# Performance work log

Measured on AMD Instinct MI355X. Metric: run time of the kernel, lower is better.

The kernel has to match this reference:

```python
import jax, jax.numpy as jnp
from jax import lax
import numpy as np

DN = ('NCHW', 'OIHW', 'NCHW')

def _conv(x, w, b):
    y = lax.conv_general_dilated(x, w, (1, 1), 'VALID', dimension_numbers=DN)
    return y + b[None, :, None, None]

def _prelu(x, a):
    return jnp.where(x >= 0, x, a[None, :, None, None] * x)

def _maxpool2(x):
    # MaxPool2d(2,2,ceil_mode=True); spatial dims chosen even so VALID matches.
    return lax.reduce_window(x, -jnp.inf, lax.max, (1, 1, 2, 2), (1, 1, 2, 2), 'VALID')

def setup_inputs() -> dict:
    key = jax.random.key(0)
    ks = jax.random.split(key, 16)
    f = jnp.float32
    x = jax.random.uniform(ks[0], (16, 3, 720, 720), dtype=f) * 255.0
    def w(k, shape, fan_in):
        return jax.random.normal(k, shape, dtype=f) * (1.0 / np.sqrt(fan_in))
    return {
        'x': x,
        'conv1_w': w(ks[1], (10, 3, 3, 3), 27), 'conv1_b': jnp.zeros((10,), f),
        'prelu1_a': jnp.full((10,), 0.25, f),
        'conv2_w': w(ks[2], (16, 10, 3, 3), 90), 'conv2_b': jnp.zeros((16,), f),
        'prelu2_a': jnp.full((16,), 0.25, f),
        'conv3_w': w(ks[3], (32, 16, 3, 3), 144), 'conv3_b': jnp.zeros((32,), f),
        'prelu3_a': jnp.full((32,), 0.25, f),
        'conv41_w': w(ks[4], (2, 32, 1, 1), 32), 'conv41_b': jnp.zeros((2,), f),
        'conv42_w': w(ks[5], (4, 32, 1, 1), 32), 'conv42_b': jnp.zeros((4,), f),
    }

def reference(x, conv1_w, conv1_b, prelu1_a, conv2_w, conv2_b, prelu2_a,
              conv3_w, conv3_b, prelu3_a, conv41_w, conv41_b, conv42_w, conv42_b):
    # MTCNN pixel normalization from detect_p_net
    h = (x - 127.5) * 0.0078125
    h = _prelu(_conv(h, conv1_w, conv1_b), prelu1_a)   # [B,10,718,718]
    h = _maxpool2(h)                                   # [B,10,359,359]
    h = _prelu(_conv(h, conv2_w, conv2_b), prelu2_a)   # [B,16,357,357]
    h = _prelu(_conv(h, conv3_w, conv3_b), prelu3_a)   # [B,32,355,355]
    prob = jax.nn.softmax(_conv(h, conv41_w, conv41_b), axis=1)  # [B,2,355,355]
    reg = _conv(h, conv42_w, conv42_b)                            # [B,4,355,355]
    return (reg, prob)
```

## Files before the change

### kernel.cpp

```cpp
#include <hip/hip_runtime.h>
#include <hip/hip_bf16.h>
#include <cstddef>


#define H1 718
#define PH 359
#define H2 357
#define H3 355

#define W1R_OFF 0
#define B1R_OFF 288
#define AW2_OFF 320
#define BW3_OFF 1600
#define P16_OFF 4096
#define C2H_OFF 16500864

typedef short bf16x8 __attribute__((ext_vector_type(8)));
typedef float f32x4  __attribute__((ext_vector_type(4)));
typedef float f32x16 __attribute__((ext_vector_type(16)));
typedef unsigned short ushort4v __attribute__((ext_vector_type(4)));

__global__ void repack_kernel(const float* __restrict__ w1, const float* __restrict__ b1,
                              const float* __restrict__ w2, const float* __restrict__ w3,
                              float* __restrict__ ws) {
    int t = threadIdx.x;
    const float S = 0.0078125f;
    for (int i = t; i < 270; i += blockDim.x) ws[W1R_OFF + i] = w1[i] * S;
    if (t < 10) {
        float s = 0.f;
        for (int i = 0; i < 27; i++) s += w1[t * 27 + i];
        ws[B1R_OFF + t] = b1[t] - 127.5f * S * s;
    }
    unsigned short* aw2 = (unsigned short*)(ws + AW2_OFF);
    for (int e = t; e < 2560; e += blockDim.x) {
        int s = e >> 9;
        int rem = e & 511;
        int l = rem >> 3, j = rem & 7;
        int q = l >> 4, co = l & 15;
        int tap = 2 * s + (q >> 1);
        int ci  = ((q & 1) << 3) + j;
        float v = (tap < 9 && ci < 10) ? w2[co * 90 + ci * 9 + tap] : 0.f;
        __hip_bfloat16 h = __float2bfloat16(v);
        aw2[e] = *(unsigned short*)&h;
    }
    unsigned short* bw3 = (unsigned short*)(ws + BW3_OFF);
    for (int e = t; e < 4608; e += blockDim.x) {
        int tap = e >> 9;
        int rem = e & 511;
        int l = rem >> 3, j = rem & 7;
        int kh = tap / 3, kw = tap % 3;
        int co = l & 31, ci = ((l >> 5) << 3) + j;
        float v = w3[co * 144 + ci * 9 + kh * 3 + kw];
        __hip_bfloat16 h = __float2bfloat16(v);
        bw3[e] = *(unsigned short*)&h;
    }
}

__global__ void conv1_pool_kernel(const float* __restrict__ x,
                                  const float* __restrict__ ws,
                                  const float* __restrict__ a1,
                                  __hip_bfloat16* __restrict__ p16) {
    int pw = blockIdx.x * blockDim.x + threadIdx.x;
    int ph = blockIdx.y;
    int n  = blockIdx.z;
    if (pw >= PH) return;
    int iy = 2 * ph, ix = 2 * pw;

    float acc[10][4];
    #pragma unroll
    for (int c = 0; c < 10; c++)
        #pragma unroll
        for (int p = 0; p < 4; p++) acc[c][p] = 0.f;

    #pragma unroll
    for (int ci = 0; ci < 3; ci++) {
        const float* xp = x + (((size_t)(n * 3 + ci) * 720 + iy) * 720 + ix);
        float win[4][4];
        #pragma unroll
        for (int r = 0; r < 4; r++) {
            float2 v0 = *(const float2*)(xp + r * 720);
            float2 v1 = *(const float2*)(xp + r * 720 + 2);
            win[r][0] = v0.x; win[r][1] = v0.y; win[r][2] = v1.x; win[r][3] = v1.y;
        }
        #pragma unroll
        for (int c = 0; c < 10; c++) {
            const float* wk = ws + W1R_OFF + c * 27 + ci * 9;
            #pragma unroll
            for (int kh = 0; kh < 3; kh++)
                #pragma unroll
                for (int kw = 0; kw < 3; kw++) {
                    float wv = wk[kh * 3 + kw];
                    acc[c][0] = fmaf(win[kh    ][kw    ], wv, acc[c][0]);
                    acc[c][1] = fmaf(win[kh    ][kw + 1], wv, acc[c][1]);
                    acc[c][2] = fmaf(win[kh + 1][kw    ], wv, acc[c][2]);
                    acc[c][3] = fmaf(win[kh + 1][kw + 1], wv, acc[c][3]);
                }
        }
    }

    __hip_bfloat16 o[16];
    #pragma unroll
    for (int c = 0; c < 10; c++) {
        float b = ws[B1R_OFF + c], al = a1[c];
        float s0 = acc[c][0] + b, s1 = acc[c][1] + b;
        float s2 = acc[c][2] + b, s3 = acc[c][3] + b;
        s0 = s0 >= 0.f ? s0 : al * s0;
        s1 = s1 >= 0.f ? s1 : al * s1;
        s2 = s2 >= 0.f ? s2 : al * s2;
        s3 = s3 >= 0.f ? s3 : al * s3;
        o[c] = __float2bfloat16(fmaxf(fmaxf(s0, s1), fmaxf(s2, s3)));
    }
    #pragma unroll
    for (int c = 10; c < 16; c++) o[c] = __float2bfloat16(0.f);

    float4* dst = (float4*)(p16 + (((size_t)n * PH + ph) * PH + pw) * 16);
    dst[0] = ((float4*)o)[0];
    dst[1] = ((float4*)o)[1];
}

__global__ __launch_bounds__(256)
void conv2_mfma_kernel(const __hip_bfloat16* __restrict__ p16,
                       const float* __restrict__ ws,
                       const float* __restrict__ b2,
                       const float* __restrict__ a2,
                       __hip_bfloat16* __restrict__ c2h) {
    int wv = threadIdx.x >> 6;
    int l  = threadIdx.x & 63;
    int oh  = blockIdx.y * 4 + wv;
    int ow0 = blockIdx.x * 64;
    int n   = blockIdx.z;
    if (oh >= H2) return;

    int pxl = l & 15;
    int q   = l >> 4;
    int taph = q >> 1;
    int choff = (q & 1) << 3;

    const bf16x8* aw = (const bf16x8*)(ws + AW2_OFF);
    bf16x8 afr[5];
    #pragma unroll
    for (int s = 0; s < 5; s++) afr[s] = aw[s * 64 + l];

    bf16x8 zf;
    #pragma unroll
    for (int j = 0; j < 8; j++) zf[j] = 0;

    f32x4 acc[4];
    #pragma unroll
    for (int t = 0; t < 4; t++)
        #pragma unroll
        for (int i = 0; i < 4; i++) acc[t][i] = 0.f;

    #pragma unroll
    for (int s = 0; s < 5; s++) {
        int tap = 2 * s + taph;
        bool real = (tap < 9);
        int kh = tap / 3, kw = tap - kh * 3;
        int ih = oh + kh; if (ih > PH - 1) ih = PH - 1;
        #pragma unroll
        for (int t = 0; t < 4; t++) {
            int iw = ow0 + t * 16 + pxl + kw; if (iw > PH - 1) iw = PH - 1;
            const bf16x8* bp = (const bf16x8*)(p16 + (((size_t)n * PH + ih) * PH + iw) * 16 + choff);
            bf16x8 b = real ? *bp : zf;
            acc[t] = __builtin_amdgcn_mfma_f32_16x16x32_bf16(afr[s], b, acc[t], 0, 0, 0);
        }
    }

    float bb[4], aa[4];
    #pragma unroll
    for (int r = 0; r < 4; r++) { bb[r] = b2[q * 4 + r]; aa[r] = a2[q * 4 + r]; }

    #pragma unroll
    for (int t = 0; t < 4; t++) {
        int px = ow0 + t * 16 + pxl;
        if (px < H2) {
            ushort4v pk;
            #pragma unroll
            for (int r = 0; r < 4; r++) {
                float v = acc[t][r] + bb[r];
                v = v >= 0.f ? v : aa[r] * v;
                __hip_bfloat16 h = __float2bfloat16(v);
                pk[r] = *(unsigned short*)&h;
            }
            *(ushort4v*)(c2h + (((size_t)n * H2 + oh) * H2 + px) * 16 + q * 4) = pk;
        }
    }
}

__global__ __launch_bounds__(256, 1)
void conv3_heads_kernel(const __hip_bfloat16* __restrict__ c2h,
                        const float* __restrict__ ws,
                        const float* __restrict__ b3,
                        const float* __restrict__ a3,
                        const float* __restrict__ w41,
                        const float* __restrict__ b41,
                        const float* __restrict__ w42,
                        const float* __restrict__ b42,
                        float* __restrict__ out) {
    int wv = threadIdx.x >> 6;
    int l  = threadIdx.x & 63;
    int ow0 = blockIdx.x * 32;
    int oh0 = blockIdx.y * 8 + wv * 2;
    int n   = blockIdx.z;

    int m    = l & 31;
    int half = l >> 5;
    int choff = half << 3;

    const bf16x8* bw = (const bf16x8*)(ws + BW3_OFF);
    bf16x8 bfr[9];
    #pragma unroll
    for (int t = 0; t < 9; t++) bfr[t] = bw[t * 64 + l];

    f32x16 acc0, acc1;
    #pragma unroll
    for (int i = 0; i < 16; i++) { acc0[i] = 0.f; acc1[i] = 0.f; }

    #pragma unroll
    for (int kh = 0; kh < 3; kh++) {
        int ih0 = oh0 + kh;     if (ih0 > H2 - 1) ih0 = H2 - 1;
        int ih1 = oh0 + 1 + kh; if (ih1 > H2 - 1) ih1 = H2 - 1;
        #pragma unroll
        for (int kw = 0; kw < 3; kw++) {
            int iw = ow0 + m + kw; if (iw > H2 - 1) iw = H2 - 1;
            const bf16x8* a0p = (const bf16x8*)(c2h + ((((size_t)n * H2 + ih0) * H2 + iw) << 4) + choff);
            const bf16x8* a1p = (const bf16x8*)(c2h + ((((size_t)n * H2 + ih1) * H2 + iw) << 4) + choff);
            bf16x8 a0 = *a0p;
            bf16x8 a1 = *a1p;
            int tap = kh * 3 + kw;
            acc0 = __builtin_amdgcn_mfma_f32_32x32x16_bf16(a0, bfr[tap], acc0, 0, 0, 0);
            acc1 = __builtin_amdgcn_mfma_f32_32x32x16_bf16(a1, bfr[tap], acc1, 0, 0, 0);
        }
    }

    __shared__ float hbuf[4][64 * 33];
    float* hb = hbuf[wv];
    float bb = b3[m], aa = a3[m];
    #pragma unroll
    for (int t = 0; t < 2; t++) {
        #pragma unroll
        for (int r = 0; r < 16; r++) {
            int mprime = (r & 3) + ((r >> 2) << 3) + (half << 2);
            float v = (t ? acc1[r] : acc0[r]) + bb;
            v = v >= 0.f ? v : aa * v;
            hb[(t * 32 + mprime) * 33 + m] = v;
        }
    }
    __syncthreads();

    int poh = oh0 + (l >> 5);
    int pow_ = ow0 + (l & 31);
    float h[32];
    #pragma unroll
    for (int c = 0; c < 32; c++) h[c] = hb[l * 33 + c];

    float l0 = b41[0], l1 = b41[1];
    float r0 = b42[0], r1 = b42[1], r2 = b42[2], r3 = b42[3];
    #pragma unroll
    for (int c = 0; c < 32; c++) {
        float hv = h[c];
        l0 = fmaf(hv, w41[c],      l0);
        l1 = fmaf(hv, w41[32 + c], l1);
        r0 = fmaf(hv, w42[c],      r0);
        r1 = fmaf(hv, w42[32 + c], r1);
        r2 = fmaf(hv, w42[64 + c], r2);
        r3 = fmaf(hv, w42[96 + c], r3);
    }
    float mx  = fmaxf(l0, l1);
    float e0 = __expf(l0 - mx), e1 = __expf(l1 - mx);
    float inv = 1.0f / (e0 + e1);

    if (poh < H3 && pow_ < H3) {
        const size_t sp = (size_t)H3 * H3;
        size_t pos = (size_t)poh * H3 + pow_;
        float* reg  = out;
        float* prob = out + (size_t)16 * 4 * sp;
        reg[((size_t)(n * 4 + 0)) * sp + pos] = r0;
        reg[((size_t)(n * 4 + 1)) * sp + pos] = r1;
        reg[((size_t)(n * 4 + 2)) * sp + pos] = r2;
        reg[((size_t)(n * 4 + 3)) * sp + pos] = r3;
        prob[((size_t)(n * 2 + 0)) * sp + pos] = e0 * inv;
        prob[((size_t)(n * 2 + 1)) * sp + pos] = e1 * inv;
    }
}

extern "C" void kernel_launch(void* const* d_in, const int* in_sizes, int n_in,
                              void* d_out, int out_size, void* d_ws, size_t ws_size,
                              hipStream_t stream) {
    const float* x   = (const float*)d_in[0];
    const float* w1  = (const float*)d_in[1];
    const float* b1  = (const float*)d_in[2];
    const float* a1  = (const float*)d_in[3];
    const float* w2  = (const float*)d_in[4];
    const float* b2  = (const float*)d_in[5];
    const float* a2  = (const float*)d_in[6];
    const float* w3  = (const float*)d_in[7];
    const float* b3  = (const float*)d_in[8];
    const float* a3  = (const float*)d_in[9];
    const float* w41 = (const float*)d_in[10];
    const float* b41 = (const float*)d_in[11];
    const float* w42 = (const float*)d_in[12];
    const float* b42 = (const float*)d_in[13];
    float* out = (float*)d_out;
    float* ws  = (float*)d_ws;

    __hip_bfloat16* p16 = (__hip_bfloat16*)(ws + P16_OFF);
    __hip_bfloat16* c2h = (__hip_bfloat16*)(ws + C2H_OFF);

    repack_kernel<<<1, 256, 0, stream>>>(w1, b1, w2, w3, ws);

    {
        dim3 grid((PH + 127) / 128, PH, 16);
        conv1_pool_kernel<<<grid, 128, 0, stream>>>(x, ws, a1, p16);
    }
    {
        dim3 grid((H2 + 63) / 64, (H2 + 3) / 4, 16);
        conv2_mfma_kernel<<<grid, 256, 0, stream>>>(p16, ws, b2, a2, c2h);
    }
    {
        dim3 grid((H3 + 31) / 32, (H3 + 7) / 8, 16);
        conv3_heads_kernel<<<grid, 256, 0, stream>>>(c2h, ws, b3, a3,
                                                     w41, b41, w42, b42, out);
    }
}
```

Before: 316.6 us.

## Run conv1+PReLU+maxpool on bf16 MFMA with LDS-staged input tile

Replaces the per-thread scalar-FMA conv1/PReLU/pool kernel with a tiled kernel. Each block stages a 66x18 input tile into shared memory, converting the three channels to bf16. It then computes the 3x3 conv as nine 32x32x16 bf16 MFMAs per row pair, using pre-scaled bf16 weights from an extended repack. PReLU and 2x2 max-pooling are fused in registers. The aim is to move conv1 off the vector ALUs. In exchange, most of the MFMA K and N lanes are padding, the raw pixel input is rounded to bf16, and outputs are written as scattered 2-byte stores. The padding channels 10-15 of the pooled buffer are also no longer explicitly zeroed.

Measured after the change: 348.6 us. 10.1% more time.

```diff
diff --git a/kernel.cpp b/kernel.cpp
--- a/kernel.cpp
+++ b/kernel.cpp
@@ -8,28 +8,43 @@
 #define H2 357
 #define H3 355
 
-#define W1R_OFF 0
-#define B1R_OFF 288
-#define AW2_OFF 320
-#define BW3_OFF 1600
-#define P16_OFF 4096
-#define C2H_OFF 16500864
+#define B1R_OFF 0
+#define BW1_OFF 16
+#define AW2_OFF 2320
+#define BW3_OFF 3600
+#define P16_OFF 5952
+#define C2H_OFF 16502720
 
 typedef short bf16x8 __attribute__((ext_vector_type(8)));
 typedef float f32x4  __attribute__((ext_vector_type(4)));
 typedef float f32x16 __attribute__((ext_vector_type(16)));
 typedef unsigned short ushort4v __attribute__((ext_vector_type(4)));
+
+static __device__ __forceinline__ bf16x8 make_a(uint2 q) {
+    union { unsigned int u[4]; bf16x8 v; } c;
+    c.u[0] = q.x; c.u[1] = q.y; c.u[2] = q.x; c.u[3] = q.y;
+    return c.v;
+}
 
 __global__ void repack_kernel(const float* __restrict__ w1, const float* __restrict__ b1,
                               const float* __restrict__ w2, const float* __restrict__ w3,
                               float* __restrict__ ws) {
     int t = threadIdx.x;
     const float S = 0.0078125f;
-    for (int i = t; i < 270; i += blockDim.x) ws[W1R_OFF + i] = w1[i] * S;
     if (t < 10) {
         float s = 0.f;
         for (int i = 0; i < 27; i++) s += w1[t * 27 + i];
         ws[B1R_OFF + t] = b1[t] - 127.5f * S * s;
+    }
+    unsigned short* bw1 = (unsigned short*)(ws + BW1_OFF);
+    for (int e = t; e < 4608; e += blockDim.x) {
+        int tap = e >> 9;
+        int rem = e & 511;
+        int l = rem >> 3, j = rem & 7;
+        int n = l & 31, k = ((l >> 5) << 3) + j;
+        float v = (k < 3 && n < 10) ? w1[n * 27 + k * 9 + tap] * S : 0.f;
+        __hip_bfloat16 h = __float2bfloat16(v);
+        bw1[e] = *(unsigned short*)&h;
     }
     unsigned short* aw2 = (unsigned short*)(ws + AW2_OFF);
     for (int e = t; e < 2560; e += blockDim.x) {
@@ -56,66 +71,82 @@
     }
 }
 
-__global__ void conv1_pool_kernel(const float* __restrict__ x,
-                                  const float* __restrict__ ws,
-                                  const float* __restrict__ a1,
-                                  __hip_bfloat16* __restrict__ p16) {
-    int pw = blockIdx.x * blockDim.x + threadIdx.x;
-    int ph = blockIdx.y;
+__global__ __launch_bounds__(256)
+void conv1_mfma_kernel(const float* __restrict__ x,
+                       const float* __restrict__ ws,
+                       const float* __restrict__ a1,
+                       __hip_bfloat16* __restrict__ p16) {
+    __shared__ uint2 st[18][68];
+    int tid = threadIdx.x;
+    int wv = tid >> 6;
+    int l  = tid & 63;
+    int x0 = blockIdx.x * 64;
+    int y0 = blockIdx.y * 16;
     int n  = blockIdx.z;
-    if (pw >= PH) return;
-    int iy = 2 * ph, ix = 2 * pw;
-
-    float acc[10][4];
-    #pragma unroll
-    for (int c = 0; c < 10; c++)
-        #pragma unroll
-        for (int p = 0; p < 4; p++) acc[c][p] = 0.f;
-
-    #pragma unroll
-    for (int ci = 0; ci < 3; ci++) {
-        const float* xp = x + (((size_t)(n * 3 + ci) * 720 + iy) * 720 + ix);
-        float win[4][4];
-        #pragma unroll
-        for (int r = 0; r < 4; r++) {
-            float2 v0 = *(const float2*)(xp + r * 720);
-            float2 v1 = *(const float2*)(xp + r * 720 + 2);
-            win[r][0] = v0.x; win[r][1] = v0.y; win[r][2] = v1.x; win[r][3] = v1.y;
-        }
-        #pragma unroll
-        for (int c = 0; c < 10; c++) {
-            const float* wk = ws + W1R_OFF + c * 27 + ci * 9;
+
+    for (int e = tid; e < 66 * 18; e += 256) {
+        int row = e / 66, xx = e - row * 66;
+        int gx = x0 + xx; if (gx > 719) gx = 719;
+        int gy = y0 + row; if (gy > 719) gy = 719;
+        const float* xp = x + (size_t)n * 1555200 + (size_t)gy * 720 + gx;
+        __hip_bfloat16 h0 = __float2bfloat16(xp[0]);
+        __hip_bfloat16 h1 = __float2bfloat16(xp[518400]);
+        __hip_bfloat16 h2 = __float2bfloat16(xp[1036800]);
+        uint2 val;
+        val.x = (unsigned int)(*(unsigned short*)&h0) |
+                ((unsigned int)(*(unsigned short*)&h1) << 16);
+        val.y = (unsigned int)(*(unsigned short*)&h2);
+        st[row][xx] = val;
+    }
+    __syncthreads();
+
+    const bf16x8* bw = (const bf16x8*)(ws + BW1_OFF);
+    bf16x8 bfr[9];
+    #pragma unroll
+    for (int t = 0; t < 9; t++) bfr[t] = bw[t * 64 + l];
+
+    int lm = l & 31, half = l >> 5;
+    float bch = (lm < 10) ? ws[B1R_OFF + lm] : 0.f;
+    float ach = (lm < 10) ? a1[lm] : 0.f;
+
+    #pragma unroll
+    for (int pr = 0; pr < 2; pr++) {
+        int ly  = (wv << 2) + (pr << 1);
+        int phg = (y0 + ly) >> 1;
+        #pragma unroll
+        for (int t = 0; t < 2; t++) {
+            f32x16 acc0, acc1;
             #pragma unroll
-            for (int kh = 0; kh < 3; kh++)
+            for (int i = 0; i < 16; i++) { acc0[i] = 0.f; acc1[i] = 0.f; }
+            int bx = (t << 5) + lm;
+            #pragma unroll
+            for (int tap = 0; tap < 9; tap++) {
+                int kh = tap / 3, kw = tap - kh * 3;
+                uint2 q0 = st[ly + kh][bx + kw];
+                uint2 q1 = st[ly + kh + 1][bx + kw];
+                acc0 = __builtin_amdgcn_mfma_f32_32x32x16_bf16(make_a(q0), bfr[tap], acc0, 0, 0, 0);
+                acc1 = __builtin_amdgcn_mfma_f32_32x32x16_bf16(make_a(q1), bfr[tap], acc1, 0, 0, 0);
+            }
+            float pv[16];
+            #pragma unroll
+            for (int r = 0; r < 16; r++) {
+                float v0 = acc0[r] + bch; v0 = fmaxf(v0, ach * v0);
+                float v1 = acc1[r] + bch; v1 = fmaxf(v1, ach * v1);
+                pv[r] = fmaxf(v0, v1);
+            }
+            if (lm < 10 && phg < PH) {
+                size_t rowbase = (((size_t)n * PH + phg) * PH) * 16 + lm;
                 #pragma unroll
-                for (int kw = 0; kw < 3; kw++) {
-                    float wv = wk[kh * 3 + kw];
-                    acc[c][0] = fmaf(win[kh    ][kw    ], wv, acc[c][0]);
-                    acc[c][1] = fmaf(win[kh    ][kw + 1], wv, acc[c][1]);
-                    acc[c][2] = fmaf(win[kh + 1][kw    ], wv, acc[c][2]);
-                    acc[c][3] = fmaf(win[kh + 1][kw + 1], wv, acc[c][3]);
+                for (int q = 0; q < 8; q++) {
+                    float pm = fmaxf(pv[2 * q], pv[2 * q + 1]);
+                    int pmi = (q & 1) + ((q >> 1) << 2) + (half << 1);
+                    int pw  = (x0 >> 1) + (t << 4) + pmi;
+                    if (pw < PH)
+                        p16[rowbase + (size_t)pw * 16] = __float2bfloat16(pm);
                 }
-        }
-    }
-
-    __hip_bfloat16 o[16];
-    #pragma unroll
-    for (int c = 0; c < 10; c++) {
-        float b = ws[B1R_OFF + c], al = a1[c];
-        float s0 = acc[c][0] + b, s1 = acc[c][1] + b;
-        float s2 = acc[c][2] + b, s3 = acc[c][3] + b;
-        s0 = s0 >= 0.f ? s0 : al * s0;
-        s1 = s1 >= 0.f ? s1 : al * s1;
-        s2 = s2 >= 0.f ? s2 : al * s2;
-        s3 = s3 >= 0.f ? s3 : al * s3;
-        o[c] = __float2bfloat16(fmaxf(fmaxf(s0, s1), fmaxf(s2, s3)));
-    }
-    #pragma unroll
-    for (int c = 10; c < 16; c++) o[c] = __float2bfloat16(0.f);
-
-    float4* dst = (float4*)(p16 + (((size_t)n * PH + ph) * PH + pw) * 16);
-    dst[0] = ((float4*)o)[0];
-    dst[1] = ((float4*)o)[1];
+            }
+        }
+    }
 }
 
 __global__ __launch_bounds__(256)
@@ -310,8 +341,8 @@
     repack_kernel<<<1, 256, 0, stream>>>(w1, b1, w2, w3, ws);
 
     {
-        dim3 grid((PH + 127) / 128, PH, 16);
-        conv1_pool_kernel<<<grid, 128, 0, stream>>>(x, ws, a1, p16);
+        dim3 grid((H1 + 63) / 64, (H1 + 15) / 16, 16);
+        conv1_mfma_kernel<<<grid, 256, 0, stream>>>(x, ws, a1, p16);
     }
     {
         dim3 grid((H2 + 63) / 64, (H2 + 3) / 4, 16);
```
